# Performance work log

Measured on AMD Instinct MI355X. Metric: run time of the kernel, lower is better.

## Reference

```python
import jax, jax.numpy as jnp
import numpy as np


def setup_inputs() -> dict:
    key = jax.random.key(0)
    k1, k2, k3, k4, k5 = jax.random.split(key, 5)
    B, N, C = 16, 131072, 2
    return {
        "r": jax.random.normal(k1, (B, N, C), dtype=jnp.float32),
        "w": jax.random.uniform(k2, (B, N, 2), dtype=jnp.float32),
        "J_p": jax.random.normal(k3, (B, N, C, 6), dtype=jnp.float32),
        "J_d": jax.random.normal(k4, (B, N, C, 1), dtype=jnp.float32),
        "lmbda": jax.random.uniform(k5, (B, 1, 1), dtype=jnp.float32),
        "iter_idx": 1,
    }


def reference(r, w, J_p, J_d, lmbda, iter_idx):
    B, N, C = r.shape
    eye6 = jnp.eye(6, dtype=r.dtype)

    safe_lmbda = jnp.where(jnp.isnan(lmbda), jnp.asarray(100.0, r.dtype), lmbda)
    safe_lmbda = jnp.maximum(safe_lmbda, 0.001)  # (B,1,1)

    conf = w[..., 0:1][..., None]                 # (B,N,1,1)
    node_lambda = w[..., 1:2]                     # (B,N,1)
    cJp = conf * J_p                              # (B,N,C,6)
    cJd = conf * J_d                              # (B,N,C,1)
    cr = w[..., 0:1] * r                          # (B,N,C)

    H_pp = jnp.einsum('bncp,bncq->bpq', J_p, cJp)            # (B,6,6)
    H_pd = jnp.einsum('bncp,bncd->bnpd', J_p, cJd)           # (B,N,6,1)
    H_dd = jnp.sum(J_d * cJd, axis=2)                        # (B,N,1)
    g_p = jnp.einsum('bncp,bnc->bp', J_p, cr)[..., None]     # (B,6,1)
    g_d = jnp.sum(J_d * cr[..., None], axis=2)               # (B,N,1)

    H_pp = H_pp + safe_lmbda * eye6[None]
    H_dd_safe = jnp.maximum(H_dd + safe_lmbda + node_lambda + 1e-4, 1e-4)
    inv_H_dd = 1.0 / H_dd_safe                    # (B,N,1)

    H_pd_invHdd = H_pd * inv_H_dd[..., None]      # (B,N,6,1)
    term_to_sub = jnp.einsum('bnpd,bnqd->bpq', H_pd_invHdd, H_pd)   # (B,6,6)
    H_eff = H_pp - term_to_sub
    g_eff = g_p - jnp.sum(H_pd_invHdd * g_d[..., None], axis=1)     # (B,6,1)

    if iter_idx >= 2:
        g_eff = g_eff.at[:, 3:].set(0.0)
        H_eff = H_eff.at[:, 3:, 3:].add(1e8)

    H_eff = H_eff + 1.0 * eye6[None]
    diag = jnp.diagonal(H_eff, axis1=-2, axis2=-1)            # (B,6)
    H_eff = H_eff + eye6[None] * (0.01 * diag)[:, :, None]

    delta_pose = jnp.linalg.solve(H_eff, g_eff)               # (B,6,1)
    v = jnp.einsum('bnpd,bp->bnd', H_pd, delta_pose[..., 0])  # (B,N,1)
    delta_depth = inv_H_dd * (g_d - v)                        # (B,N,1)

    delta_pose = jnp.clip(delta_pose[..., 0], -2.0, 2.0)      # (B,6)
    delta_depth = jnp.clip(delta_depth, -5.0, 5.0)
    delta_pose = jnp.where(jnp.any(jnp.isnan(delta_pose)), jnp.zeros_like(delta_pose), delta_pose)
    delta_depth = jnp.where(jnp.any(jnp.isnan(delta_depth)), jnp.zeros_like(delta_depth), delta_depth)
    return (delta_pose, delta_depth)
```

## Files before the change

### kernel.cpp

```cpp
#include <hip/hip_runtime.h>
#include <math.h>

#define BATCH 16
#define NPB 131072
#define BLOCKS_PER_B 64
#define THREADS 256
#define PPT (NPB / (BLOCKS_PER_B * THREADS))
#define NACC 27

__device__ __forceinline__ float safe_lambda(float l) {
    if (isnan(l)) l = 100.0f;
    return fmaxf(l, 0.001f);
}

struct Pt { float4 a0, a1, a2; float2 jd, rv, wv; };

__device__ __forceinline__ void load_pt(const float* __restrict__ Jp, const float* __restrict__ Jd,
                                        const float* __restrict__ r, const float* __restrict__ w,
                                        long n, Pt& P)
{
    const float4* jp4 = (const float4*)(Jp + n * 12);
    P.a0 = jp4[0]; P.a1 = jp4[1]; P.a2 = jp4[2];
    P.jd = *(const float2*)(Jd + n * 2);
    P.rv = *(const float2*)(r  + n * 2);
    P.wv = *(const float2*)(w  + n * 2);
}

__device__ __forceinline__ void acc_pt(const Pt& P, float lam, float (&D)[21], float (&G)[6])
{
    float jp[12] = {P.a0.x, P.a0.y, P.a0.z, P.a0.w,
                    P.a1.x, P.a1.y, P.a1.z, P.a1.w,
                    P.a2.x, P.a2.y, P.a2.z, P.a2.w};
    const float conf = P.wv.x, nl = P.wv.y;
    const float jdx = P.jd.x, jdy = P.jd.y;
    const float rx  = P.rv.x, ry  = P.rv.y;

    float h[6], hi[6];
#pragma unroll
    for (int p = 0; p < 6; ++p) h[p] = conf * (jp[p] * jdx + jp[6 + p] * jdy);
    const float Hdd = conf * (jdx * jdx + jdy * jdy);
    const float gd  = conf * (jdx * rx + jdy * ry);
    const float inv = 1.0f / fmaxf(Hdd + lam + nl + 1e-4f, 1e-4f);
#pragma unroll
    for (int p = 0; p < 6; ++p) hi[p] = h[p] * inv;

    int idx = 0;
#pragma unroll
    for (int p = 0; p < 6; ++p) {
#pragma unroll
        for (int q = p; q < 6; ++q) {
            D[idx] += conf * (jp[p] * jp[q] + jp[6 + p] * jp[6 + q]) - hi[p] * h[q];
            ++idx;
        }
    }
#pragma unroll
    for (int p = 0; p < 6; ++p)
        G[p] += conf * (jp[p] * rx + jp[6 + p] * ry) - hi[p] * gd;
}

__global__ __launch_bounds__(THREADS, 2) void dba_pass1(
    const float* __restrict__ r, const float* __restrict__ w,
    const float* __restrict__ Jp, const float* __restrict__ Jd,
    const float* __restrict__ lmbda, float* __restrict__ partials)
{
    const int b   = blockIdx.y;
    const int blk = blockIdx.x;
    const int t   = threadIdx.x;
    const float lam = safe_lambda(lmbda[b]);

    float D[21], G[6];
#pragma unroll
    for (int i = 0; i < 21; ++i) D[i] = 0.0f;
#pragma unroll
    for (int i = 0; i < 6; ++i) G[i] = 0.0f;

    const long base = (long)b * NPB + (long)blk * (THREADS * PPT) + t;

    Pt A, B;
    load_pt(Jp, Jd, r, w, base + 0 * THREADS, A);
#pragma unroll
    for (int it = 0; it < PPT; it += 2) {
        load_pt(Jp, Jd, r, w, base + (it + 1) * THREADS, B);
        acc_pt(A, lam, D, G);
        if (it + 2 < PPT)
            load_pt(Jp, Jd, r, w, base + (it + 2) * THREADS, A);
        acc_pt(B, lam, D, G);
    }

#pragma unroll
    for (int i = 0; i < 21; ++i) {
        float v = D[i];
        v += __shfl_xor(v, 1);  v += __shfl_xor(v, 2);  v += __shfl_xor(v, 4);
        v += __shfl_xor(v, 8);  v += __shfl_xor(v, 16); v += __shfl_xor(v, 32);
        D[i] = v;
    }
#pragma unroll
    for (int i = 0; i < 6; ++i) {
        float v = G[i];
        v += __shfl_xor(v, 1);  v += __shfl_xor(v, 2);  v += __shfl_xor(v, 4);
        v += __shfl_xor(v, 8);  v += __shfl_xor(v, 16); v += __shfl_xor(v, 32);
        G[i] = v;
    }

    __shared__ float s_red[4][NACC];
    const int wid  = t >> 6;
    const int lane = t & 63;
    if (lane == 0) {
#pragma unroll
        for (int i = 0; i < 21; ++i) s_red[wid][i] = D[i];
#pragma unroll
        for (int i = 0; i < 6; ++i)  s_red[wid][21 + i] = G[i];
    }
    __syncthreads();
    if (t < NACC) {
        float v = s_red[0][t] + s_red[1][t] + s_red[2][t] + s_red[3][t];
        partials[((long)b * NACC + t) * BLOCKS_PER_B + blk] = v;
    }
}

__global__ void dba_solve(
    const float* __restrict__ partials, const float* __restrict__ lmbda,
    const int* __restrict__ iter_idx,
    float* __restrict__ out_pose,
    float* __restrict__ dp_raw)
{
    const int b = blockIdx.x;
    const int t = threadIdx.x;
    __shared__ float s[NACC];
    if (t < NACC) {
        const float4* p4 = (const float4*)(partials + ((long)b * NACC + t) * BLOCKS_PER_B);
        float4 a = make_float4(0.f, 0.f, 0.f, 0.f);
#pragma unroll
        for (int k = 0; k < BLOCKS_PER_B / 4; ++k) {
            float4 v = p4[k];
            a.x += v.x; a.y += v.y; a.z += v.z; a.w += v.w;
        }
        s[t] = (a.x + a.y) + (a.z + a.w);
    }
    __syncthreads();
    if (t != 0) return;

    const float lam = safe_lambda(lmbda[b]);
    float H[6][6], g[6];
    int idx = 0;
    for (int p = 0; p < 6; ++p)
        for (int q = p; q < 6; ++q) {
            float v = s[idx];
            H[p][q] = v; H[q][p] = v;
            idx++;
        }
    for (int p = 0; p < 6; ++p) g[p] = s[21 + p];
    for (int p = 0; p < 6; ++p) H[p][p] += lam;

    if (*iter_idx >= 2) {
        for (int p = 3; p < 6; ++p) g[p] = 0.0f;
        for (int p = 3; p < 6; ++p)
            for (int q = 3; q < 6; ++q) H[p][q] += 1e8f;
    }
    for (int p = 0; p < 6; ++p) H[p][p] += 1.0f;
    for (int p = 0; p < 6; ++p) H[p][p] += 0.01f * H[p][p];

    float A[6][7];
    for (int p = 0; p < 6; ++p) {
        for (int q = 0; q < 6; ++q) A[p][q] = H[p][q];
        A[p][6] = g[p];
    }
    for (int col = 0; col < 6; ++col) {
        int piv = col; float best = fabsf(A[col][col]);
        for (int rr = col + 1; rr < 6; ++rr) {
            float v = fabsf(A[rr][col]);
            if (v > best) { best = v; piv = rr; }
        }
        if (piv != col)
            for (int cc = col; cc < 7; ++cc) {
                float tmp = A[col][cc]; A[col][cc] = A[piv][cc]; A[piv][cc] = tmp;
            }
        const float invp = 1.0f / A[col][col];
        for (int rr = col + 1; rr < 6; ++rr) {
            const float f = A[rr][col] * invp;
            for (int cc = col; cc < 7; ++cc) A[rr][cc] -= f * A[col][cc];
        }
    }
    float x[6];
    for (int rr = 5; rr >= 0; --rr) {
        float v = A[rr][6];
        for (int cc = rr + 1; cc < 6; ++cc) v -= A[rr][cc] * x[cc];
        x[rr] = v / A[rr][rr];
    }
    for (int p = 0; p < 6; ++p) {
        dp_raw[b * 6 + p] = x[p];
        out_pose[b * 6 + p] = fminf(fmaxf(x[p], -2.0f), 2.0f);
    }
}

__device__ __forceinline__ float depth_pt(const Pt& P, float lam, const float (&dp)[6])
{
    float jp[12] = {P.a0.x, P.a0.y, P.a0.z, P.a0.w,
                    P.a1.x, P.a1.y, P.a1.z, P.a1.w,
                    P.a2.x, P.a2.y, P.a2.z, P.a2.w};
    const float conf = P.wv.x, nl = P.wv.y;
    const float jdx = P.jd.x, jdy = P.jd.y;
    const float rx  = P.rv.x, ry  = P.rv.y;

    float v = 0.0f;
#pragma unroll
    for (int p = 0; p < 6; ++p) {
        const float h = conf * (jp[p] * jdx + jp[6 + p] * jdy);
        v += h * dp[p];
    }
    const float Hdd = conf * (jdx * jdx + jdy * jdy);
    const float gd  = conf * (jdx * rx + jdy * ry);
    const float inv = 1.0f / fmaxf(Hdd + lam + nl + 1e-4f, 1e-4f);
    float dd = inv * (gd - v);
    return fminf(fmaxf(dd, -5.0f), 5.0f);
}

__global__ __launch_bounds__(THREADS) void dba_pass3(
    const float* __restrict__ r, const float* __restrict__ w,
    const float* __restrict__ Jp, const float* __restrict__ Jd,
    const float* __restrict__ lmbda, const float* __restrict__ dp_raw,
    float* __restrict__ out_dd)
{
    const int b   = blockIdx.y;
    const int blk = blockIdx.x;
    const int t   = threadIdx.x;
    const float lam = safe_lambda(lmbda[b]);

    float dp[6];
#pragma unroll
    for (int p = 0; p < 6; ++p) dp[p] = dp_raw[b * 6 + p];

    const long base = (long)b * NPB + (long)blk * (THREADS * PPT) + t;

    Pt A, B;
    load_pt(Jp, Jd, r, w, base + 0 * THREADS, A);
#pragma unroll
    for (int it = 0; it < PPT; it += 2) {
        load_pt(Jp, Jd, r, w, base + (it + 1) * THREADS, B);
        out_dd[base + it * THREADS] = depth_pt(A, lam, dp);
        if (it + 2 < PPT)
            load_pt(Jp, Jd, r, w, base + (it + 2) * THREADS, A);
        out_dd[base + (it + 1) * THREADS] = depth_pt(B, lam, dp);
    }
}

extern "C" void kernel_launch(void* const* d_in, const int* in_sizes, int n_in,
                              void* d_out, int out_size, void* d_ws, size_t ws_size,
                              hipStream_t stream) {
    const float* r     = (const float*)d_in[0];
    const float* w     = (const float*)d_in[1];
    const float* Jp    = (const float*)d_in[2];
    const float* Jd    = (const float*)d_in[3];
    const float* lmbda = (const float*)d_in[4];
    const int*   iter  = (const int*)  d_in[5];

    float* out      = (float*)d_out;
    float* partials = (float*)d_ws;
    float* dp_raw   = partials + (long)BATCH * NACC * BLOCKS_PER_B;

    dim3 grid(BLOCKS_PER_B, BATCH);
    dba_pass1<<<grid, THREADS, 0, stream>>>(r, w, Jp, Jd, lmbda, partials);
    dba_solve<<<BATCH, 64, 0, stream>>>(partials, lmbda, iter, out, dp_raw);
    dba_pass3<<<grid, THREADS, 0, stream>>>(r, w, Jp, Jd, lmbda, dp_raw, out + BATCH * 6);
}
```

Measured before the change: 59.36 us.

## Cache per-point Schur terms in workspace so the depth pass skips reloading inputs

The first pass now writes each point's scaled H_pd/H_dd terms and g_d/H_dd into two float4 workspace arrays. A new lightweight depth kernel reads only those 32 bytes per point, instead of re-reading the 72 bytes of Jacobians, residuals and weights and recomputing. This cuts HBM traffic in the memory-bound third pass but adds write traffic to the first pass and needs a large workspace. If the workspace is too small, it falls back to the old path. The accumulation arithmetic is also reorganised around precomputed conf*Jp products with separate FMAs.

```diff
diff --git a/kernel.cpp b/kernel.cpp
--- a/kernel.cpp
+++ b/kernel.cpp
@@ -7,6 +7,12 @@
 #define THREADS 256
 #define PPT (NPB / (BLOCKS_PER_B * THREADS))
 #define NACC 27
+#define NPTS ((long)BATCH * NPB)
+
+#define WS_PARTIALS_F ((long)BATCH * NACC * BLOCKS_PER_B)
+#define WS_DPRAW_F    ((long)BATCH * 6)
+#define WS_HEAD_F     (WS_PARTIALS_F + WS_DPRAW_F)
+#define WS_NEEDED_B   ((WS_HEAD_F + NPTS * 8) * 4)
 
 __device__ __forceinline__ float safe_lambda(float l) {
     if (isnan(l)) l = 100.0f;
@@ -26,7 +32,9 @@
     P.wv = *(const float2*)(w  + n * 2);
 }
 
-__device__ __forceinline__ void acc_pt(const Pt& P, float lam, float (&D)[21], float (&G)[6])
+template<bool STORE>
+__device__ __forceinline__ void acc_pt(const Pt& P, float lam, float (&D)[21], float (&G)[6],
+                                       float4* __restrict__ sA, float4* __restrict__ sB, long n)
 {
     float jp[12] = {P.a0.x, P.a0.y, P.a0.z, P.a0.w,
                     P.a1.x, P.a1.y, P.a1.z, P.a1.w,
@@ -35,33 +43,49 @@
     const float jdx = P.jd.x, jdy = P.jd.y;
     const float rx  = P.rv.x, ry  = P.rv.y;
 
+    float cjp[12];
+#pragma unroll
+    for (int i = 0; i < 12; ++i) cjp[i] = conf * jp[i];
+
     float h[6], hi[6];
 #pragma unroll
-    for (int p = 0; p < 6; ++p) h[p] = conf * (jp[p] * jdx + jp[6 + p] * jdy);
+    for (int p = 0; p < 6; ++p) h[p] = cjp[p] * jdx + cjp[6 + p] * jdy;
     const float Hdd = conf * (jdx * jdx + jdy * jdy);
     const float gd  = conf * (jdx * rx + jdy * ry);
     const float inv = 1.0f / fmaxf(Hdd + lam + nl + 1e-4f, 1e-4f);
 #pragma unroll
     for (int p = 0; p < 6; ++p) hi[p] = h[p] * inv;
 
+    if (STORE) {
+        sA[n] = make_float4(hi[0], hi[1], hi[2], hi[3]);
+        sB[n] = make_float4(hi[4], hi[5], gd * inv, 0.0f);
+    }
+
     int idx = 0;
 #pragma unroll
     for (int p = 0; p < 6; ++p) {
 #pragma unroll
         for (int q = p; q < 6; ++q) {
-            D[idx] += conf * (jp[p] * jp[q] + jp[6 + p] * jp[6 + q]) - hi[p] * h[q];
+            D[idx] += cjp[p] * jp[q];
+            D[idx] += cjp[6 + p] * jp[6 + q];
+            D[idx] -= hi[p] * h[q];
             ++idx;
         }
     }
 #pragma unroll
-    for (int p = 0; p < 6; ++p)
-        G[p] += conf * (jp[p] * rx + jp[6 + p] * ry) - hi[p] * gd;
-}
-
+    for (int p = 0; p < 6; ++p) {
+        G[p] += cjp[p] * rx;
+        G[p] += cjp[6 + p] * ry;
+        G[p] -= hi[p] * gd;
+    }
+}
+
+template<bool STORE>
 __global__ __launch_bounds__(THREADS, 2) void dba_pass1(
     const float* __restrict__ r, const float* __restrict__ w,
     const float* __restrict__ Jp, const float* __restrict__ Jd,
-    const float* __restrict__ lmbda, float* __restrict__ partials)
+    const float* __restrict__ lmbda, float* __restrict__ partials,
+    float4* __restrict__ sA, float4* __restrict__ sB)
 {
     const int b   = blockIdx.y;
     const int blk = blockIdx.x;
@@ -81,10 +105,10 @@
 #pragma unroll
     for (int it = 0; it < PPT; it += 2) {
         load_pt(Jp, Jd, r, w, base + (it + 1) * THREADS, B);
-        acc_pt(A, lam, D, G);
+        acc_pt<STORE>(A, lam, D, G, sA, sB, base + it * THREADS);
         if (it + 2 < PPT)
             load_pt(Jp, Jd, r, w, base + (it + 2) * THREADS, A);
-        acc_pt(B, lam, D, G);
+        acc_pt<STORE>(B, lam, D, G, sA, sB, base + (it + 1) * THREADS);
     }
 
 #pragma unroll
@@ -190,6 +214,36 @@
     for (int p = 0; p < 6; ++p) {
         dp_raw[b * 6 + p] = x[p];
         out_pose[b * 6 + p] = fminf(fmaxf(x[p], -2.0f), 2.0f);
+    }
+}
+
+__global__ __launch_bounds__(THREADS) void dba_pass3_fast(
+    const float4* __restrict__ sA, const float4* __restrict__ sB,
+    const float* __restrict__ dp_raw, float* __restrict__ out_dd)
+{
+    const int b   = blockIdx.y;
+    const int blk = blockIdx.x;
+    const int t   = threadIdx.x;
+
+    float dp[6];
+#pragma unroll
+    for (int p = 0; p < 6; ++p) dp[p] = dp_raw[b * 6 + p];
+
+    const long base = (long)b * NPB + (long)blk * (THREADS * PPT) + t;
+
+#pragma unroll
+    for (int it = 0; it < PPT; ++it) {
+        const long n = base + (long)it * THREADS;
+        float4 a = sA[n];
+        float4 c = sB[n];
+        float dd = c.z;
+        dd -= a.x * dp[0];
+        dd -= a.y * dp[1];
+        dd -= a.z * dp[2];
+        dd -= a.w * dp[3];
+        dd -= c.x * dp[4];
+        dd -= c.y * dp[5];
+        out_dd[n] = fminf(fmaxf(dd, -5.0f), 5.0f);
     }
 }
 
@@ -256,10 +310,20 @@
 
     float* out      = (float*)d_out;
     float* partials = (float*)d_ws;
-    float* dp_raw   = partials + (long)BATCH * NACC * BLOCKS_PER_B;
+    float* dp_raw   = partials + WS_PARTIALS_F;
+    float4* sA      = (float4*)((float*)d_ws + WS_HEAD_F);
+    float4* sB      = sA + NPTS;
+
+    const bool store = (ws_size >= (size_t)WS_NEEDED_B);
 
     dim3 grid(BLOCKS_PER_B, BATCH);
-    dba_pass1<<<grid, THREADS, 0, stream>>>(r, w, Jp, Jd, lmbda, partials);
-    dba_solve<<<BATCH, 64, 0, stream>>>(partials, lmbda, iter, out, dp_raw);
-    dba_pass3<<<grid, THREADS, 0, stream>>>(r, w, Jp, Jd, lmbda, dp_raw, out + BATCH * 6);
-}
+    if (store) {
+        dba_pass1<true><<<grid, THREADS, 0, stream>>>(r, w, Jp, Jd, lmbda, partials, sA, sB);
+        dba_solve<<<BATCH, 64, 0, stream>>>(partials, lmbda, iter, out, dp_raw);
+        dba_pass3_fast<<<grid, THREADS, 0, stream>>>(sA, sB, dp_raw, out + BATCH * 6);
+    } else {
+        dba_pass1<false><<<grid, THREADS, 0, stream>>>(r, w, Jp, Jd, lmbda, partials, sA, sB);
+        dba_solve<<<BATCH, 64, 0, stream>>>(partials, lmbda, iter, out, dp_raw);
+        dba_pass3<<<grid, THREADS, 0, stream>>>(r, w, Jp, Jd, lmbda, dp_raw, out + BATCH * 6);
+    }
+}
```

After: 70.32 us. +18.5%, slower.
